# Kernel tuning notes

Measured on AMD Instinct MI355X. Metric: run time of the kernel, lower is better.

Reference implementation:

```python
import jax, jax.numpy as jnp
import numpy as np

B, C, W, H = 4, 256, 64, 64
DK = C // 8  # query/key channels


def setup_inputs() -> dict:
    key = jax.random.key(0)
    ks = jax.random.split(key, 7)
    x = jax.random.normal(ks[0], (B, C, W, H), dtype=jnp.float32)
    # conv1x1 weights stored as [out_ch, in_ch]
    Wq = jax.random.normal(ks[1], (DK, C), dtype=jnp.float32) / np.sqrt(C)
    bq = jnp.zeros((DK,), dtype=jnp.float32)
    Wk = jax.random.normal(ks[2], (DK, C), dtype=jnp.float32) / np.sqrt(C)
    bk = jnp.zeros((DK,), dtype=jnp.float32)
    Wv = jax.random.normal(ks[3], (C, C), dtype=jnp.float32) / np.sqrt(C)
    bv = jnp.zeros((C,), dtype=jnp.float32)
    gamma = jnp.zeros((1,), dtype=jnp.float32)
    return {"x": x, "Wq": Wq, "bq": bq, "Wk": Wk, "bk": bk,
            "Wv": Wv, "bv": bv, "gamma": gamma}


def reference(x, Wq, bq, Wk, bk, Wv, bv, gamma):
    b, c, w, h = x.shape
    n = w * h
    xf = x.reshape(b, c, n)                     # [B, C, N]
    # conv1x1 == channel matmul
    q = jnp.einsum('dc,bcn->bnd', Wq, xf) + bq  # [B, N, DK]
    k = jnp.einsum('dc,bcn->bdn', Wk, xf) + bk[None, :, None]  # [B, DK, N]
    energy = jnp.einsum('bnd,bdm->bnm', q, k)   # [B, N, N]
    attention = jax.nn.softmax(energy, axis=-1)
    v = jnp.einsum('dc,bcn->bdn', Wv, xf) + bv[None, :, None]  # [B, C, N]
    out = jnp.einsum('bdm,bnm->bdn', v, attention)              # [B, C, N]
    out = out.reshape(b, c, w, h)
    out = gamma * out + x
    return out, attention
```

## Files before the change

kernel.cpp:

```cpp
#include <hip/hip_runtime.h>
#include <hip/hip_bf16.h>

typedef __attribute__((ext_vector_type(8))) short bf16x8;
typedef __attribute__((ext_vector_type(4))) float f32x4;
typedef __attribute__((ext_vector_type(4))) unsigned int u32x4;
typedef __attribute__((ext_vector_type(2))) unsigned int u32x2;

#define B_SZ 4
#define C_SZ 256
#define N_SZ 4096
#define DK_SZ 32

#define WQB_OFF 0
#define WKB_OFF 8192
#define WVB_OFF 16384
#define QB_OFF  81920
#define KB_OFF  606208
#define VB_OFF  1130496

__device__ __forceinline__ short f2bf(float f) {
    union { float f; unsigned int u; } v; v.f = f;
    unsigned int r = v.u + 0x7fffu + ((v.u >> 16) & 1u);
    return (short)(r >> 16);
}

__device__ __forceinline__ unsigned int cvt_pk_bf16(float lo, float hi) {
    unsigned int r;
    asm volatile("v_cvt_pk_bf16_f32 %0, %1, %2" : "=v"(r) : "v"(lo), "v"(hi));
    return r;
}

__device__ __forceinline__ f32x4 mfma16(bf16x8 a, bf16x8 b, f32x4 c) {
    return __builtin_amdgcn_mfma_f32_16x16x32_bf16(a, b, c, 0, 0, 0);
}

__device__ __forceinline__ void gload_lds16(const void* g, void* l) {
    __builtin_amdgcn_global_load_lds((const __attribute__((address_space(1))) unsigned int*)g,
                                     (__attribute__((address_space(3))) unsigned int*)l, 16, 0, 0);
}

__global__ __launch_bounds__(256) void k_convw(const float* __restrict__ Wq,
                                               const float* __restrict__ Wk,
                                               const float* __restrict__ Wv,
                                               short* __restrict__ ws) {
    int i = blockIdx.x * 256 + threadIdx.x;
    if (i < 8192) {
        ws[WQB_OFF + i] = f2bf(Wq[i]);
        ws[WKB_OFF + i] = f2bf(Wk[i]);
    }
    ws[WVB_OFF + i] = f2bf(Wv[i]);
}

__global__ __launch_bounds__(256) void k_prep(const float* __restrict__ x,
                                              const float* __restrict__ bq,
                                              const float* __restrict__ bk,
                                              const float* __restrict__ bv,
                                              short* __restrict__ ws) {
    __shared__ short xsT[64][264];
    __shared__ short vt_s[64][258];

    const int b = blockIdx.y;
    const int n0 = blockIdx.x * 64;
    const int t = threadIdx.x;
    const float* xb = x + (size_t)b * C_SZ * N_SZ;

    {
        int c0 = t >> 4, n4 = (t & 15) * 4;
#pragma unroll
        for (int i = 0; i < 16; i++) {
            int c = c0 + 16 * i;
            float4 v = *(const float4*)(xb + (size_t)c * N_SZ + n0 + n4);
            xsT[n4 + 0][c] = f2bf(v.x);
            xsT[n4 + 1][c] = f2bf(v.y);
            xsT[n4 + 2][c] = f2bf(v.z);
            xsT[n4 + 3][c] = f2bf(v.w);
        }
    }
    __syncthreads();

    const int w = t >> 6, l = t & 63;
    const int lr = l & 15, lk = l >> 4;

    bf16x8 af[8];
#pragma unroll
    for (int kk = 0; kk < 8; kk++)
        af[kk] = *(const bf16x8*)(&xsT[w * 16 + lr][kk * 32 + lk * 8]);

#pragma unroll
    for (int qk = 0; qk < 2; qk++) {
        const short* wb = ws + (qk ? WKB_OFF : WQB_OFF);
        const float* bias = qk ? bk : bq;
        short* outp = ws + (qk ? KB_OFF : QB_OFF) + (size_t)b * N_SZ * DK_SZ;
#pragma unroll
        for (int cf = 0; cf < 2; cf++) {
            f32x4 acc = {0.f, 0.f, 0.f, 0.f};
#pragma unroll
            for (int kk = 0; kk < 8; kk++) {
                bf16x8 bfr = *(const bf16x8*)(wb + (cf * 16 + lr) * 256 + kk * 32 + lk * 8);
                acc = mfma16(af[kk], bfr, acc);
            }
            float bias_v = bias[cf * 16 + lr];
#pragma unroll
            for (int r = 0; r < 4; r++) {
                int row = w * 16 + lk * 4 + r;
                outp[(size_t)(n0 + row) * DK_SZ + cf * 16 + lr] = f2bf(acc[r] + bias_v);
            }
        }
    }

#pragma unroll
    for (int cf = 0; cf < 16; cf++) {
        f32x4 acc = {0.f, 0.f, 0.f, 0.f};
#pragma unroll
        for (int kk = 0; kk < 8; kk++) {
            bf16x8 bfr = *(const bf16x8*)(ws + WVB_OFF + (cf * 16 + lr) * 256 + kk * 32 + lk * 8);
            acc = mfma16(af[kk], bfr, acc);
        }
        float bias_v = bv[cf * 16 + lr];
#pragma unroll
        for (int r = 0; r < 4; r++) {
            vt_s[w * 16 + lk * 4 + r][cf * 16 + lr] = f2bf(acc[r] + bias_v);
        }
    }
    __syncthreads();
    {
        short* vb = ws + VB_OFF + (size_t)b * C_SZ * N_SZ;
        int nn = t & 63;
#pragma unroll
        for (int i = 0; i < 64; i++) {
            int c = (t >> 6) + 4 * i;
            vb[(size_t)c * N_SZ + n0 + nn] = vt_s[nn][c];
        }
    }
}

__global__ __launch_bounds__(512, 2) void k_attn(const short* __restrict__ ws,
                                                 const float* __restrict__ x,
                                                 const float* __restrict__ gamma_p,
                                                 float* __restrict__ out) {
    __shared__ short v_lds[3][256 * 64];
    __shared__ short p_lds[2][64][72];
    __shared__ float rsum_s[2][64];

    const int b = blockIdx.y;
    const int n0 = blockIdx.x * 64;
    const int t = threadIdx.x, w = t >> 6, l = t & 63;
    const int rg = w & 3, ch = w >> 2;
    const int rp = w & 1, cp = w >> 1;
    const int lr = l & 15, lk = l >> 4;

    const short* qb = ws + QB_OFF + (size_t)b * N_SZ * DK_SZ;
    const short* kb = ws + KB_OFF + (size_t)b * N_SZ * DK_SZ;
    const short* vb = ws + VB_OFF + (size_t)b * C_SZ * N_SZ;

    bf16x8 qf = *(const bf16x8*)(qb + (size_t)(n0 + rg * 16 + lr) * DK_SZ + lk * 8);

    float rs = 0.f;
    for (int mt = 0; mt < 32; mt++) {
        int mb = ch * 2048 + mt * 64;
        bf16x8 kfa = *(const bf16x8*)(kb + (size_t)(mb + lr) * DK_SZ + lk * 8);
        bf16x8 kfb = *(const bf16x8*)(kb + (size_t)(mb + 16 + lr) * DK_SZ + lk * 8);
        bf16x8 kfc = *(const bf16x8*)(kb + (size_t)(mb + 32 + lr) * DK_SZ + lk * 8);
        bf16x8 kfd = *(const bf16x8*)(kb + (size_t)(mb + 48 + lr) * DK_SZ + lk * 8);
        f32x4 s0 = mfma16(kfa, qf, (f32x4){0.f, 0.f, 0.f, 0.f});
        f32x4 s1 = mfma16(kfb, qf, (f32x4){0.f, 0.f, 0.f, 0.f});
        f32x4 s2 = mfma16(kfc, qf, (f32x4){0.f, 0.f, 0.f, 0.f});
        f32x4 s3 = mfma16(kfd, qf, (f32x4){0.f, 0.f, 0.f, 0.f});
#pragma unroll
        for (int r = 0; r < 4; r++)
            rs += __expf(s0[r]) + __expf(s1[r]) + __expf(s2[r]) + __expf(s3[r]);
    }
    rs += __shfl_xor(rs, 16);
    rs += __shfl_xor(rs, 32);
    if (l < 16) rsum_s[ch][rg * 16 + l] = rs;
    __syncthreads();
    const float invp = 1.f / (rsum_s[0][rg * 16 + lr] + rsum_s[1][rg * 16 + lr]);

    float* attn_row = out + (size_t)B_SZ * C_SZ * N_SZ + (size_t)b * N_SZ * N_SZ
                      + (size_t)(n0 + rg * 16 + lr) * N_SZ;
    f32x4 O[2][4];
#pragma unroll
    for (int rf = 0; rf < 2; rf++)
#pragma unroll
        for (int cb = 0; cb < 4; cb++) O[rf][cb] = (f32x4){0.f, 0.f, 0.f, 0.f};

    bf16x8 kf0, kf1;

#define KLOAD(tt)                                                                  \
    {                                                                              \
        const int mbase = (tt) * 64 + ch * 32;                                     \
        kf0 = *(const bf16x8*)(kb + (size_t)(mbase + lr) * DK_SZ + lk * 8);        \
        kf1 = *(const bf16x8*)(kb + (size_t)(mbase + 16 + lr) * DK_SZ + lk * 8);   \
    }

#define STAGE(tt, vbuf)                                                            \
    {                                                                              \
        const int mb = (tt) * 64;                                                  \
        _Pragma("unroll")                                                          \
        for (int i = 0; i < 4; i++) {                                              \
            int c = w * 32 + i * 8 + (l >> 3);                                     \
            int j = l & 7;                                                         \
            const short* g = vb + (size_t)c * N_SZ + mb + ((j ^ (c & 7)) << 3);    \
            gload_lds16(g, (void*)&v_lds[vbuf][(w * 32 + i * 8) * 64]);            \
        }                                                                          \
    }

#define SCOMP(tt, pb)                                                              \
    {                                                                              \
        const int mbase = (tt) * 64 + ch * 32;                                     \
        f32x4 s0 = mfma16(kf0, qf, (f32x4){0.f, 0.f, 0.f, 0.f});                   \
        f32x4 s1 = mfma16(kf1, qf, (f32x4){0.f, 0.f, 0.f, 0.f});                   \
        f32x4 e0, e1;                                                              \
        e0[0] = __expf(s0[0]) * invp; e0[1] = __expf(s0[1]) * invp;                \
        e0[2] = __expf(s0[2]) * invp; e0[3] = __expf(s0[3]) * invp;                \
        e1[0] = __expf(s1[0]) * invp; e1[1] = __expf(s1[1]) * invp;                \
        e1[2] = __expf(s1[2]) * invp; e1[3] = __expf(s1[3]) * invp;                \
        __builtin_nontemporal_store(e0, (f32x4*)(attn_row + mbase + lk * 4));      \
        __builtin_nontemporal_store(e1, (f32x4*)(attn_row + mbase + 16 + lk * 4)); \
        u32x2 pk0, pk1;                                                            \
        pk0[0] = cvt_pk_bf16(e0[0], e0[1]); pk0[1] = cvt_pk_bf16(e0[2], e0[3]);    \
        pk1[0] = cvt_pk_bf16(e1[0], e1[1]); pk1[1] = cvt_pk_bf16(e1[2], e1[3]);    \
        *(u32x2*)(&p_lds[pb][rg * 16 + lr][ch * 32 + lk * 4]) = pk0;               \
        *(u32x2*)(&p_lds[pb][rg * 16 + lr][ch * 32 + 16 + lk * 4]) = pk1;          \
    }

    KLOAD(0);
    __builtin_amdgcn_sched_barrier(0);
    STAGE(0, 0);
    STAGE(1, 1);
    __builtin_amdgcn_sched_barrier(0);
    SCOMP(0, 0);

    for (int mt = 0; mt < 64; mt++) {
        asm volatile("s_waitcnt vmcnt(6) lgkmcnt(0)" ::: "memory");
        __builtin_amdgcn_sched_barrier(0);
        __builtin_amdgcn_s_barrier();
        __builtin_amdgcn_sched_barrier(0);
        const int cur = mt & 1;
        if (mt < 63) {
            KLOAD(mt + 1);
            __builtin_amdgcn_sched_barrier(0);
            if (mt < 62) STAGE(mt + 2, (mt + 2) % 3);
            __builtin_amdgcn_sched_barrier(0);
            SCOMP(mt + 1, cur ^ 1);
        }
        const int vcur = mt % 3;
        const char* pbase = (const char*)&p_lds[cur][rp * 32 + lr][0];
        bf16x8 a00 = *(const bf16x8*)(pbase + lk * 16);
        bf16x8 a01 = *(const bf16x8*)(pbase + 64 + lk * 16);
        bf16x8 a10 = *(const bf16x8*)(pbase + 2304 + lk * 16);
        bf16x8 a11 = *(const bf16x8*)(pbase + 2304 + 64 + lk * 16);
        const char* vbase = (const char*)&v_lds[vcur][0];
#pragma unroll
        for (int cb = 0; cb < 4; cb++) {
            int c = cp * 64 + cb * 16 + lr;
            int sw = (c & 7) << 4;
            bf16x8 b0 = *(const bf16x8*)(vbase + c * 128 + ((lk << 4) ^ sw));
            bf16x8 b1 = *(const bf16x8*)(vbase + c * 128 + (((4 + lk) << 4) ^ sw));
            O[0][cb] = mfma16(a00, b0, O[0][cb]);
            O[0][cb] = mfma16(a01, b1, O[0][cb]);
            O[1][cb] = mfma16(a10, b0, O[1][cb]);
            O[1][cb] = mfma16(a11, b1, O[1][cb]);
        }
    }
#undef KLOAD
#undef STAGE
#undef SCOMP

    __syncthreads();
    const float g = gamma_p[0];
    float* o_s = (float*)&v_lds[0][0];
    const float* xb = x + (size_t)b * C_SZ * N_SZ;
    float* ob = out + (size_t)b * C_SZ * N_SZ;
#pragma unroll
    for (int half = 0; half < 2; half++) {
        if (rp == half) {
#pragma unroll
            for (int rf = 0; rf < 2; rf++)
#pragma unroll
                for (int cb = 0; cb < 4; cb++)
#pragma unroll
                    for (int r = 0; r < 4; r++)
                        o_s[(rf * 16 + lk * 4 + r) * 258 + cp * 64 + cb * 16 + lr] = O[rf][cb][r];
        }
        __syncthreads();
        {
            int nn = t & 31;
            int c0 = t >> 5;
#pragma unroll
            for (int i = 0; i < 16; i++) {
                int c = c0 + 16 * i;
                size_t idx = (size_t)c * N_SZ + n0 + half * 32 + nn;
                ob[idx] = g * o_s[nn * 258 + c] + xb[idx];
            }
        }
        __syncthreads();
    }
}

extern "C" void kernel_launch(void* const* d_in, const int* in_sizes, int n_in,
                              void* d_out, int out_size, void* d_ws, size_t ws_size,
                              hipStream_t stream) {
    const float* x     = (const float*)d_in[0];
    const float* Wq    = (const float*)d_in[1];
    const float* bq    = (const float*)d_in[2];
    const float* Wk    = (const float*)d_in[3];
    const float* bk    = (const float*)d_in[4];
    const float* Wv    = (const float*)d_in[5];
    const float* bv    = (const float*)d_in[6];
    const float* gamma = (const float*)d_in[7];
    short* ws = (short*)d_ws;
    float* out = (float*)d_out;

    hipLaunchKernelGGL(k_convw, dim3(256), dim3(256), 0, stream, Wq, Wk, Wv, ws);
    hipLaunchKernelGGL(k_prep, dim3(64, 4), dim3(256), 0, stream, x, bq, bk, bv, ws);
    hipLaunchKernelGGL(k_attn, dim3(64, 4), dim3(512), 0, stream, ws, x, gamma, out);
}
```

Measured before the change: 155.3 us.

## Stage K tiles through LDS and reorder attention pipeline stores

K tiles for the second pass are now fetched asynchronously into a triple-buffered LDS array alongside V, instead of being loaded directly into registers. The score/exp computation is split from the nontemporal attention stores, and the stores are issued after the next prefetch so they overlap with the MFMA work. The wait count and barriers are retuned to match. Blocks are remapped onto a 1D grid that interleaves batches, probably to spread work across XCDs and caches. The occupancy hint drops to one block per CU, and the extra LDS use could limit occupancy.

```diff
diff --git a/kernel.cpp b/kernel.cpp
--- a/kernel.cpp
+++ b/kernel.cpp
@@ -37,6 +37,11 @@
 __device__ __forceinline__ void gload_lds16(const void* g, void* l) {
     __builtin_amdgcn_global_load_lds((const __attribute__((address_space(1))) unsigned int*)g,
                                      (__attribute__((address_space(3))) unsigned int*)l, 16, 0, 0);
+}
+
+__device__ __forceinline__ void remap_block(int i, int& b, int& n0) {
+    b = (i & 7) >> 1;
+    n0 = (((i >> 3) << 1) | (i & 1)) * 64;
 }
 
 __global__ __launch_bounds__(256) void k_convw(const float* __restrict__ Wq,
@@ -59,8 +64,8 @@
     __shared__ short xsT[64][264];
     __shared__ short vt_s[64][258];
 
-    const int b = blockIdx.y;
-    const int n0 = blockIdx.x * 64;
+    int b, n0;
+    remap_block(blockIdx.x, b, n0);
     const int t = threadIdx.x;
     const float* xb = x + (size_t)b * C_SZ * N_SZ;
 
@@ -134,16 +139,17 @@
     }
 }
 
-__global__ __launch_bounds__(512, 2) void k_attn(const short* __restrict__ ws,
+__global__ __launch_bounds__(512, 1) void k_attn(const short* __restrict__ ws,
                                                  const float* __restrict__ x,
                                                  const float* __restrict__ gamma_p,
                                                  float* __restrict__ out) {
-    __shared__ short v_lds[3][256 * 64];
+    __shared__ short v_lds[3][16384];
+    __shared__ short k_lds[3][2304];
     __shared__ short p_lds[2][64][72];
     __shared__ float rsum_s[2][64];
 
-    const int b = blockIdx.y;
-    const int n0 = blockIdx.x * 64;
+    int b, n0;
+    remap_block(blockIdx.x, b, n0);
     const int t = threadIdx.x, w = t >> 6, l = t & 63;
     const int rg = w & 3, ch = w >> 2;
     const int rp = w & 1, cp = w >> 1;
@@ -152,6 +158,7 @@
     const short* qb = ws + QB_OFF + (size_t)b * N_SZ * DK_SZ;
     const short* kb = ws + KB_OFF + (size_t)b * N_SZ * DK_SZ;
     const short* vb = ws + VB_OFF + (size_t)b * C_SZ * N_SZ;
+    const char* kbb = (const char*)kb;
 
     bf16x8 qf = *(const bf16x8*)(qb + (size_t)(n0 + rg * 16 + lr) * DK_SZ + lk * 8);
 
@@ -184,39 +191,35 @@
 #pragma unroll
         for (int cb = 0; cb < 4; cb++) O[rf][cb] = (f32x4){0.f, 0.f, 0.f, 0.f};
 
-    bf16x8 kf0, kf1;
-
-#define KLOAD(tt)                                                                  \
+    f32x4 e0, e1;
+    int sc_mbase = 0;
+
+#define STAGE(tt, buf)                                                             \
     {                                                                              \
-        const int mbase = (tt) * 64 + ch * 32;                                     \
-        kf0 = *(const bf16x8*)(kb + (size_t)(mbase + lr) * DK_SZ + lk * 8);        \
-        kf1 = *(const bf16x8*)(kb + (size_t)(mbase + 16 + lr) * DK_SZ + lk * 8);   \
-    }
-
-#define STAGE(tt, vbuf)                                                            \
-    {                                                                              \
+        gload_lds16(kbb + (size_t)(tt) * 4096 + w * 512 + l * 16,                  \
+                    (void*)&k_lds[buf][w * 256]);                                  \
         const int mb = (tt) * 64;                                                  \
         _Pragma("unroll")                                                          \
         for (int i = 0; i < 4; i++) {                                              \
             int c = w * 32 + i * 8 + (l >> 3);                                     \
             int j = l & 7;                                                         \
             const short* g = vb + (size_t)c * N_SZ + mb + ((j ^ (c & 7)) << 3);    \
-            gload_lds16(g, (void*)&v_lds[vbuf][(w * 32 + i * 8) * 64]);            \
+            gload_lds16(g, (void*)&v_lds[buf][(w * 32 + i * 8) * 64]);             \
         }                                                                          \
     }
 
-#define SCOMP(tt, pb)                                                              \
+#define SCOMP_CALC(tt, pb)                                                         \
     {                                                                              \
-        const int mbase = (tt) * 64 + ch * 32;                                     \
+        sc_mbase = (tt) * 64 + ch * 32;                                            \
+        const char* kl = (const char*)&k_lds[(tt) % 3][0];                         \
+        bf16x8 kf0 = *(const bf16x8*)(kl + (ch * 32 + lr) * 64 + lk * 16);         \
+        bf16x8 kf1 = *(const bf16x8*)(kl + (ch * 32 + 16 + lr) * 64 + lk * 16);    \
         f32x4 s0 = mfma16(kf0, qf, (f32x4){0.f, 0.f, 0.f, 0.f});                   \
         f32x4 s1 = mfma16(kf1, qf, (f32x4){0.f, 0.f, 0.f, 0.f});                   \
-        f32x4 e0, e1;                                                              \
         e0[0] = __expf(s0[0]) * invp; e0[1] = __expf(s0[1]) * invp;                \
         e0[2] = __expf(s0[2]) * invp; e0[3] = __expf(s0[3]) * invp;                \
         e1[0] = __expf(s1[0]) * invp; e1[1] = __expf(s1[1]) * invp;                \
         e1[2] = __expf(s1[2]) * invp; e1[3] = __expf(s1[3]) * invp;                \
-        __builtin_nontemporal_store(e0, (f32x4*)(attn_row + mbase + lk * 4));      \
-        __builtin_nontemporal_store(e1, (f32x4*)(attn_row + mbase + 16 + lk * 4)); \
         u32x2 pk0, pk1;                                                            \
         pk0[0] = cvt_pk_bf16(e0[0], e0[1]); pk0[1] = cvt_pk_bf16(e0[2], e0[3]);    \
         pk1[0] = cvt_pk_bf16(e1[0], e1[1]); pk1[1] = cvt_pk_bf16(e1[2], e1[3]);    \
@@ -224,26 +227,32 @@
         *(u32x2*)(&p_lds[pb][rg * 16 + lr][ch * 32 + 16 + lk * 4]) = pk1;          \
     }
 
-    KLOAD(0);
-    __builtin_amdgcn_sched_barrier(0);
+#define SSTORE()                                                                   \
+    {                                                                              \
+        __builtin_nontemporal_store(e0, (f32x4*)(attn_row + sc_mbase + lk * 4));   \
+        __builtin_nontemporal_store(e1, (f32x4*)(attn_row + sc_mbase + 16 + lk * 4)); \
+    }
+
     STAGE(0, 0);
     STAGE(1, 1);
     __builtin_amdgcn_sched_barrier(0);
-    SCOMP(0, 0);
+    asm volatile("s_waitcnt vmcnt(9)" ::: "memory");
+    __builtin_amdgcn_sched_barrier(0);
+    SCOMP_CALC(0, 0);
+    SSTORE();
 
     for (int mt = 0; mt < 64; mt++) {
-        asm volatile("s_waitcnt vmcnt(6) lgkmcnt(0)" ::: "memory");
+        asm volatile("s_waitcnt vmcnt(2) lgkmcnt(0)" ::: "memory");
         __builtin_amdgcn_sched_barrier(0);
         __builtin_amdgcn_s_barrier();
         __builtin_amdgcn_sched_barrier(0);
         const int cur = mt & 1;
-        if (mt < 63) {
-            KLOAD(mt + 1);
-            __builtin_amdgcn_sched_barrier(0);
-            if (mt < 62) STAGE(mt + 2, (mt + 2) % 3);
-            __builtin_amdgcn_sched_barrier(0);
-            SCOMP(mt + 1, cur ^ 1);
-        }
+        if (mt < 63) SCOMP_CALC(mt + 1, cur ^ 1);
+        __builtin_amdgcn_sched_barrier(0);
+        if (mt < 62) STAGE(mt + 2, (mt + 2) % 3);
+        __builtin_amdgcn_sched_barrier(0);
+        if (mt < 63) SSTORE();
+        __builtin_amdgcn_sched_barrier(0);
         const int vcur = mt % 3;
         const char* pbase = (const char*)&p_lds[cur][rp * 32 + lr][0];
         bf16x8 a00 = *(const bf16x8*)(pbase + lk * 16);
@@ -263,9 +272,9 @@
             O[1][cb] = mfma16(a11, b1, O[1][cb]);
         }
     }
-#undef KLOAD
 #undef STAGE
-#undef SCOMP
+#undef SCOMP_CALC
+#undef SSTORE
 
     __syncthreads();
     const float g = gamma_p[0];
@@ -313,6 +322,6 @@
     float* out = (float*)d_out;
 
     hipLaunchKernelGGL(k_convw, dim3(256), dim3(256), 0, stream, Wq, Wk, Wv, ws);
-    hipLaunchKernelGGL(k_prep, dim3(64, 4), dim3(256), 0, stream, x, bq, bk, bv, ws);
-    hipLaunchKernelGGL(k_attn, dim3(64, 4), dim3(512), 0, stream, ws, x, gamma, out);
-}
+    hipLaunchKernelGGL(k_prep, dim3(256), dim3(256), 0, stream, x, bq, bk, bv, ws);
+    hipLaunchKernelGGL(k_attn, dim3(256), dim3(512), 0, stream, ws, x, gamma, out);
+}
```

Result: faster. 147.1 us (-5.3%).
